# Kernel optimization log

Measured on AMD Instinct MI355X. Metric: run time of the kernel, lower is better.

## Reference

```python
import jax, jax.numpy as jnp
import numpy as np

B, N = 256, 2000          # clouds, points per cloud
M1, M2 = 100, 5           # fps sample counts (ratio 0.05 twice)
K1, K2 = 20, 20           # neighbors per cluster (= 1/ratio)
R1, R2, R3 = 0.3, 1.0, 2.0
F1, F2, F3 = 5, 25, 45


def _fps(pts, m):
    # iterative farthest point sampling, deterministic start at index 0
    n = pts.shape[0]
    def step(carry, _):
        mind, last = carry
        d = jnp.sum((pts - pts[last]) ** 2, axis=-1)
        mind = jnp.minimum(mind, d)
        return (mind, jnp.argmax(mind).astype(jnp.int32)), last
    _, idx = jax.lax.scan(step, (jnp.full((n,), 1e10, pts.dtype), jnp.int32(0)), None, length=m)
    return idx


def _radius_knn(q, pts, k, r):
    # k nearest neighbors of each query, masked to the radius ball (static-shape gnn.radius)
    d = jnp.sum((q[:, None, :] - pts[None, :, :]) ** 2, axis=-1)  # (M, n)
    negd, idx = jax.lax.top_k(-d, k)
    return idx, (-negd) <= r * r


def _masked_max(h, mask):
    return jnp.max(jnp.where(mask[..., None], h, -1e10), axis=1)


def _forward(points, W1, b1, W2, b2, W3, b3, D1, bD1, D2, bD2, D3, bD3):
    def per_cloud(pts):
        # ---- encode level 1 ----
        samples = pts[_fps(pts, M1)]                              # (M1,3)
        idx1, m1 = _radius_knn(samples, pts, K1, R1)
        rel = (pts[idx1] - samples[:, None, :]) / R1 * m1[..., None]   # (M1,K1,3)
        f1 = _masked_max(jax.nn.relu(rel @ W1 + b1), m1)          # (M1,F1)
        # ---- encode level 2 ----
        samples2 = samples[_fps(samples, M2)]                     # (M2,3)
        idx2, m2 = _radius_knn(samples2, samples, K2, R2)
        rel2 = (samples[idx2] - samples2[:, None, :]) / R2 * m2[..., None]
        h2 = jax.nn.relu(jnp.concatenate([rel2, f1[idx2]], axis=-1) @ W2 + b2)
        f2 = _masked_max(h2, m2)                                  # (M2,F2)
        # ---- encode level 3 (global) ----
        rel3 = samples2 / R3
        h3 = jax.nn.relu(jnp.concatenate([rel3, f2], axis=-1) @ W3 + b3)
        latent = jnp.max(h3, axis=0)                              # (F3,)
        # ---- hierarchical decode ----
        o1 = (latent @ D1 + bD1).reshape(M2, 3 + F2)
        dec, cf = o1[:, :3], jax.nn.relu(o1[:, 3:])               # (M2,3),(M2,F2)
        o2 = (cf @ D2 + bD2).reshape(M2 * K2, 3 + F1)
        dec2, cf2 = o2[:, :3], jax.nn.relu(o2[:, 3:])             # (M2*K2,3/F1)
        dec3 = (cf2 @ D3 + bD3).reshape(M2 * K2 * K1, 3)
        # ---- reconstruction: repeat_interleave + add + scale ----
        s2_out = dec * R3
        s_out = (jnp.repeat(s2_out, K2, axis=0) + dec2) * R2
        return (jnp.repeat(s_out, K1, axis=0) + dec3) * R1        # (N,3)
    return jax.vmap(per_cloud)(points).reshape(B * N, 3)


def setup_inputs():
    key = jax.random.key(0)
    ks = jax.random.split(key, 8)
    p = lambda k, s: jax.random.normal(k, s, jnp.float32) * 0.1
    z = lambda s: jnp.zeros((s,), jnp.float32)
    return {
        "points": jax.random.normal(ks[0], (B, N, 3), jnp.float32),
        "W1": p(ks[1], (3, F1)), "b1": z(F1),
        "W2": p(ks[2], (3 + F1, F2)), "b2": z(F2),
        "W3": p(ks[3], (3 + F2, F3)), "b3": z(F3),
        "D1": p(ks[4], (F3, M2 * (3 + F2))), "bD1": z(M2 * (3 + F2)),
        "D2": p(ks[5], (F2, K2 * (3 + F1))), "bD2": z(K2 * (3 + F1)),
        "D3": p(ks[6], (F1, K1 * 3)), "bD3": z(K1 * 3),
    }


def reference(points, W1, b1, W2, b2, W3, b3, D1, bD1, D2, bD2, D3, bD3):
    return _forward(points, W1, b1, W2, b2, W3, b3, D1, bD1, D2, bD2, D3, bD3)
```

## Files before the change

### kernel.cpp

```cpp
#include <hip/hip_runtime.h>

#define TPB 512
#define NW 8
#define NPTS 2000
#define M1C 100
#define M2C 5
#define KNN 20
#define CANDCAP 128

typedef float v2f __attribute__((ext_vector_type(2)));

__device__ __forceinline__ float dist3(float px, float py, float pz,
                                       float qx, float qy, float qz) {
#pragma clang fp contract(off)
    float dx = px - qx, dy = py - qy, dz = pz - qz;
    return dx * dx + dy * dy + dz * dz;
}

__device__ __forceinline__ v2f dist3p(v2f px, v2f py, v2f pz, v2f q0, v2f q1, v2f q2) {
#pragma clang fp contract(off)
    v2f dx = px - q0, dy = py - q1, dz = pz - q2;
    v2f ax = dx * dx;
    v2f ay = dy * dy;
    v2f az = dz * dz;
    return (ax + ay) + az;
}

#define ARGMAX_STEP(ctrl, rm)                                                        \
    do {                                                                             \
        float ov = __int_as_float(__builtin_amdgcn_update_dpp(                       \
            (int)0xff800000, __float_as_int(v), ctrl, rm, 0xf, false));              \
        int oi = __builtin_amdgcn_update_dpp(0x7fffffff, i, ctrl, rm, 0xf, false);   \
        bool take = (ov > v) || (ov == v && oi < i);                                 \
        v = take ? ov : v;                                                           \
        i = take ? oi : i;                                                           \
    } while (0)

__device__ __forceinline__ void wave_argmax(float& v, int& i) {
    ARGMAX_STEP(0x111, 0xf);
    ARGMAX_STEP(0x112, 0xf);
    ARGMAX_STEP(0x114, 0xf);
    ARGMAX_STEP(0x118, 0xf);
    ARGMAX_STEP(0x142, 0xa);
    ARGMAX_STEP(0x143, 0xc);
    v = __int_as_float(__builtin_amdgcn_readlane(__float_as_int(v), 63));
    i = __builtin_amdgcn_readlane(i, 63);
}

#define FMAX_STEP(ctrl, rm)                                                          \
    do {                                                                             \
        float _t = __int_as_float(__builtin_amdgcn_update_dpp(                       \
            (int)0xff800000, __float_as_int(x), ctrl, rm, 0xf, false));              \
        x = fmaxf(x, _t);                                                            \
    } while (0)

__device__ __forceinline__ float wave_fmax(float x) {
    FMAX_STEP(0x111, 0xf);
    FMAX_STEP(0x112, 0xf);
    FMAX_STEP(0x114, 0xf);
    FMAX_STEP(0x118, 0xf);
    FMAX_STEP(0x142, 0xa);
    FMAX_STEP(0x143, 0xc);
    return __int_as_float(__builtin_amdgcn_readlane(__float_as_int(x), 63));
}

__global__ __launch_bounds__(TPB, 2) void fused_kernel(
    const float* __restrict__ P,
    const float* __restrict__ W1, const float* __restrict__ b1,
    const float* __restrict__ W2, const float* __restrict__ b2,
    const float* __restrict__ W3, const float* __restrict__ b3,
    const float* __restrict__ D1, const float* __restrict__ bD1,
    const float* __restrict__ D2, const float* __restrict__ bD2,
    const float* __restrict__ D3, const float* __restrict__ bD3,
    float* __restrict__ out)
{
    __shared__ float sx[NPTS], sy[NPTS], sz[NPTS];
    __shared__ float smpx[M1C], smpy[M1C], smpz[M1C];
    __shared__ float s2x[M2C], s2y[M2C], s2z[M2C];
    __shared__ float f1s[M1C][5];
    __shared__ float knd[NW][CANDCAP];
    __shared__ int   kni[NW][CANDCAP];
    __shared__ float vin[M2C][KNN][8];
    __shared__ __align__(16) float4 sA[2][4];
    __shared__ __align__(16) float  sZ[2][4];
    __shared__ int cnt;
    __shared__ float f2s[M2C][25];
    __shared__ float latent[45];
    __shared__ float decv[M2C][3];
    __shared__ float cfs[M2C][25];
    __shared__ float dec2s[M1C][3];
    __shared__ float cf2s[M1C][5];
    __shared__ float w2s[200], b2s[25], w3s[1260], b3s[45];

    const int b = blockIdx.x;
    const int tid = threadIdx.x;
    const int lane = tid & 63;
    const int wid = tid >> 6;

    const float R1SQ = (float)(0.3 * 0.3);
    const float R2SQ = 1.0f;
    const float INVR1 = 1.0f / 0.3f;

    const float* Pb = P + (size_t)b * (NPTS * 3);
    for (int j = tid; j < NPTS; j += TPB) {
        sx[j] = Pb[3 * j + 0];
        sy[j] = Pb[3 * j + 1];
        sz[j] = Pb[3 * j + 2];
    }
    for (int t = tid; t < 200; t += TPB) w2s[t] = W2[t];
    for (int t = tid; t < 25; t += TPB) b2s[t] = b2[t];
    for (int t = tid; t < 1260; t += TPB) w3s[t] = W3[t];
    for (int t = tid; t < 45; t += TPB) b3s[t] = b3[t];
    if (tid == 0) cnt = 0;
    __syncthreads();

    if (wid < 4) {
        v2f px2[4], py2[4], pz2[4], mind2[4];
#pragma unroll
        for (int p = 0; p < 4; ++p) {
#pragma unroll
            for (int h = 0; h < 2; ++h) {
                int k = 2 * p + h;
                int j = tid + (k << 8);
                bool v = j < NPTS;
                int jc = v ? j : 0;
                px2[p][h] = v ? sx[jc] : 1e18f;
                py2[p][h] = v ? sy[jc] : 1e18f;
                pz2[p][h] = v ? sz[jc] : 1e18f;
                mind2[p][h] = v ? 1e10f : -1.0f;
            }
        }

        float qx = sx[0], qy = sy[0], qz = sz[0];
        for (int it = 0; it < M1C; ++it) {
            if (tid == 0) { smpx[it] = qx; smpy[it] = qy; smpz[it] = qz; }
            v2f q0 = {qx, qx}, q1 = {qy, qy}, q2 = {qz, qz};
            float m[8];
#pragma unroll
            for (int p = 0; p < 4; ++p) {
                v2f d = dist3p(px2[p], py2[p], pz2[p], q0, q1, q2);
                v2f mm;
                mm[0] = fminf(mind2[p][0], d[0]);
                mm[1] = fminf(mind2[p][1], d[1]);
                mind2[p] = mm;
                m[2 * p] = mm[0];
                m[2 * p + 1] = mm[1];
            }
            float va = m[0]; int ka = 0; if (m[1] > va) { va = m[1]; ka = 1; }
            float vb = m[2]; int kb = 2; if (m[3] > vb) { vb = m[3]; kb = 3; }
            float vc = m[4]; int kc = 4; if (m[5] > vc) { vc = m[5]; kc = 5; }
            float vd = m[6]; int kd = 6; if (m[7] > vd) { vd = m[7]; kd = 7; }
            if (vb > va) { va = vb; ka = kb; }
            if (vd > vc) { vc = vd; kc = kd; }
            if (vc > va) { va = vc; ka = kc; }
            float bv = va; int bi = tid + (ka << 8);
            if (it == M1C - 1) {
                if (lane == 0)
                    __hip_atomic_fetch_add(&cnt, 1, __ATOMIC_RELEASE,
                                           __HIP_MEMORY_SCOPE_WORKGROUP);
                break;
            }
            float lv = bv; int li = bi;
            wave_argmax(bv, bi);
            int p = it & 1;
            if (lv == bv && li == bi) {
                int k = bi >> 8;
                float cx = px2[0][0], cy = py2[0][0], cz = pz2[0][0];
#pragma unroll
                for (int kk = 1; kk < 8; ++kk) {
                    bool t = (k == kk);
                    cx = t ? px2[kk >> 1][kk & 1] : cx;
                    cy = t ? py2[kk >> 1][kk & 1] : cy;
                    cz = t ? pz2[kk >> 1][kk & 1] : cz;
                }
                sA[p][wid] = make_float4(bv, __int_as_float(bi), cx, cy);
                sZ[p][wid] = cz;
            }
            if (lane == 0)
                __hip_atomic_fetch_add(&cnt, 1, __ATOMIC_RELEASE,
                                       __HIP_MEMORY_SCOPE_WORKGROUP);
            int need = 4 * (it + 1);
            for (;;) {
                int c = __hip_atomic_load(&cnt, __ATOMIC_ACQUIRE,
                                          __HIP_MEMORY_SCOPE_WORKGROUP);
                if (c >= need) break;
                __builtin_amdgcn_s_sleep(1);
            }
            float4 a0 = sA[p][0], a1 = sA[p][1], a2 = sA[p][2], a3 = sA[p][3];
            float4 z0 = *(const float4*)&sZ[p][0];
            float cv0 = a0.x; int ci0 = __float_as_int(a0.y);
            float x0 = a0.z, y0 = a0.w, zz0 = z0.x;
            {
                int ii = __float_as_int(a1.y);
                bool t = (a1.x > cv0) || (a1.x == cv0 && ii < ci0);
                if (t) { cv0 = a1.x; ci0 = ii; x0 = a1.z; y0 = a1.w; zz0 = z0.y; }
            }
            float cv1 = a2.x; int ci1 = __float_as_int(a2.y);
            float x1 = a2.z, y1 = a2.w, zz1 = z0.z;
            {
                int ii = __float_as_int(a3.y);
                bool t = (a3.x > cv1) || (a3.x == cv1 && ii < ci1);
                if (t) { cv1 = a3.x; ci1 = ii; x1 = a3.z; y1 = a3.w; zz1 = z0.w; }
            }
            bool t = (cv1 > cv0) || (cv1 == cv0 && ci1 < ci0);
            qx = t ? x1 : x0; qy = t ? y1 : y0; qz = t ? zz1 : zz0;
        }

        if (wid == 0) {
            float ax = smpx[lane], ay = smpy[lane], az = smpz[lane];
            bool vb2 = lane < (M1C - 64);
            float bx2 = vb2 ? smpx[lane + 64] : 1e18f;
            float by2 = vb2 ? smpy[lane + 64] : 1e18f;
            float bz2 = vb2 ? smpz[lane + 64] : 1e18f;
            float m2a = 1e10f;
            float m2b = vb2 ? 1e10f : -1.0f;
            int last2 = 0;
            for (int it = 0; it < M2C; ++it) {
                float fx = smpx[last2], fy = smpy[last2], fz = smpz[last2];
                if (lane == 0) { s2x[it] = fx; s2y[it] = fy; s2z[it] = fz; }
                m2a = fminf(m2a, dist3(ax, ay, az, fx, fy, fz));
                m2b = fminf(m2b, dist3(bx2, by2, bz2, fx, fy, fz));
                float v = m2a; int i = lane;
                if (m2b > v) { v = m2b; i = lane + 64; }
                wave_argmax(v, i);
                last2 = i;
            }
        }
    } else {
        float rw1[15], rb1[5];
#pragma unroll
        for (int i = 0; i < 15; ++i) rw1[i] = W1[i];
#pragma unroll
        for (int i = 0; i < 5; ++i) rb1[i] = b1[i];

        for (int s = wid - 4; s < M1C; s += 4) {
            while (__hip_atomic_load(&cnt, __ATOMIC_ACQUIRE,
                                     __HIP_MEMORY_SCOPE_WORKGROUP) < 4 * (s + 1))
                __builtin_amdgcn_s_sleep(2);
            float qx = smpx[s], qy = smpy[s], qz = smpz[s];
            int cn = 0;
#pragma unroll 4
            for (int c = 0; c < 32; ++c) {
                int j = c * 64 + lane;
                float d = 0.0f; bool pred = false;
                if (j < NPTS) {
                    d = dist3(sx[j], sy[j], sz[j], qx, qy, qz);
                    pred = (d <= R1SQ);
                }
                unsigned long long mb = __ballot(pred);
                if (pred) {
                    int pos = cn + (int)__popcll(mb & ((1ull << lane) - 1ull));
                    if (pos < CANDCAP) { knd[wid][pos] = d; kni[wid][pos] = j; }
                }
                cn += (int)__popcll(mb);
            }
            if (cn > CANDCAP) cn = CANDCAP;
            float fmx[5];
#pragma unroll
            for (int f = 0; f < 5; ++f) fmx[f] = -1e30f;
            for (int t = lane; t < cn; t += 64) {
                float d = knd[wid][t]; int j = kni[wid][t];
                bool valid = true;
                if (cn > KNN) {
                    int rank = 0;
                    for (int u = 0; u < cn; ++u) {
                        float du = knd[wid][u]; int iu = kni[wid][u];
                        rank += (du < d || (du == d && iu < j)) ? 1 : 0;
                    }
                    valid = rank < KNN;
                }
                if (valid) {
                    float rx = (sx[j] - qx) * INVR1;
                    float ry = (sy[j] - qy) * INVR1;
                    float rz = (sz[j] - qz) * INVR1;
#pragma unroll
                    for (int f = 0; f < 5; ++f) {
                        float h = fmaf(rx, rw1[f], fmaf(ry, rw1[5 + f], fmaf(rz, rw1[10 + f], rb1[f])));
                        fmx[f] = fmaxf(fmx[f], fmaxf(h, 0.0f));
                    }
                }
            }
#pragma unroll
            for (int f = 0; f < 5; ++f) fmx[f] = wave_fmax(fmx[f]);
            if (lane == 0) {
#pragma unroll
                for (int f = 0; f < 5; ++f) f1s[s][f] = fmx[f];
            }
        }
    }
    __syncthreads();

    for (int s = wid; s < M2C; s += NW) {
        float qx2 = s2x[s], qy2 = s2y[s], qz2 = s2z[s];
        int cn = 0;
#pragma unroll
        for (int c = 0; c < 2; ++c) {
            int j = c * 64 + lane;
            float d = 0.0f; bool pred = false;
            if (j < M1C) {
                d = dist3(smpx[j], smpy[j], smpz[j], qx2, qy2, qz2);
                pred = (d <= R2SQ);
            }
            unsigned long long mb = __ballot(pred);
            if (pred) {
                int pos = cn + (int)__popcll(mb & ((1ull << lane) - 1ull));
                knd[wid][pos] = d; kni[wid][pos] = j;
            }
            cn += (int)__popcll(mb);
        }
        int nv = 0;
#pragma unroll
        for (int c = 0; c < 2; ++c) {
            int t = c * 64 + lane;
            bool valid = false;
            float in8[8];
            if (t < cn) {
                float d = knd[wid][t]; int j = kni[wid][t];
                valid = true;
                if (cn > KNN) {
                    int rank = 0;
                    for (int u = 0; u < cn; ++u) {
                        float du = knd[wid][u]; int iu = kni[wid][u];
                        rank += (du < d || (du == d && iu < j)) ? 1 : 0;
                    }
                    valid = rank < KNN;
                }
                if (valid) {
                    in8[0] = smpx[j] - qx2; in8[1] = smpy[j] - qy2; in8[2] = smpz[j] - qz2;
#pragma unroll
                    for (int f = 0; f < 5; ++f) in8[3 + f] = f1s[j][f];
                }
            }
            unsigned long long mb = __ballot(valid);
            if (valid) {
                int pos = nv + (int)__popcll(mb & ((1ull << lane) - 1ull));
#pragma unroll
                for (int i = 0; i < 8; ++i) vin[s][pos][i] = in8[i];
            }
            nv += (int)__popcll(mb);
        }
        if (lane < 25) {
            float hmx = -1e30f;
            for (int c = 0; c < nv; ++c) {
                float h = b2s[lane];
#pragma unroll
                for (int i = 0; i < 8; ++i) h = fmaf(vin[s][c][i], w2s[i * 25 + lane], h);
                hmx = fmaxf(hmx, fmaxf(h, 0.0f));
            }
            f2s[s][lane] = hmx;
        }
    }
    __syncthreads();

    if (wid == 0 && lane < 45) {
        float lm = -1e30f;
        for (int r = 0; r < M2C; ++r) {
            float h = b3s[lane];
            h = fmaf(s2x[r] * 0.5f, w3s[0 * 45 + lane], h);
            h = fmaf(s2y[r] * 0.5f, w3s[1 * 45 + lane], h);
            h = fmaf(s2z[r] * 0.5f, w3s[2 * 45 + lane], h);
#pragma unroll
            for (int i = 0; i < 25; ++i) h = fmaf(f2s[r][i], w3s[(3 + i) * 45 + lane], h);
            lm = fmaxf(lm, fmaxf(h, 0.0f));
        }
        latent[lane] = lm;
    }
    __syncthreads();

    for (int t = tid; t < 140; t += TPB) {
        float acc = bD1[t];
        for (int i = 0; i < 45; i++) acc = fmaf(latent[i], D1[i * 140 + t], acc);
        int r = t / 28, c = t % 28;
        if (c < 3) decv[r][c] = acc;
        else cfs[r][c - 3] = fmaxf(acc, 0.0f);
    }
    __syncthreads();

    for (int t = tid; t < 800; t += TPB) {
        int r = t / 160, c = t % 160;
        float acc = bD2[c];
        for (int i = 0; i < 25; i++) acc = fmaf(cfs[r][i], D2[i * 160 + c], acc);
        int g = r * 20 + c / 8, c8 = c % 8;
        if (c8 < 3) dec2s[g][c8] = acc;
        else cf2s[g][c8 - 3] = fmaxf(acc, 0.0f);
    }
    __syncthreads();

    float* outb = out + (size_t)b * (NPTS * 3);
    for (int t = tid; t < NPTS * 3; t += TPB) {
        int n = t / 3, c = t % 3;
        int g = n / 20;
        int m = n / 400;
        int r60 = (n % 20) * 3 + c;
        float acc = bD3[r60];
        for (int i = 0; i < 5; i++) acc = fmaf(cf2s[g][i], D3[i * 60 + r60], acc);
        float val = ((decv[m][c] * 2.0f + dec2s[g][c]) + acc) * 0.3f;
        outb[t] = val;
    }
}

extern "C" void kernel_launch(void* const* d_in, const int* in_sizes, int n_in,
                              void* d_out, int out_size, void* d_ws, size_t ws_size,
                              hipStream_t stream) {
    const float* P   = (const float*)d_in[0];
    const float* W1  = (const float*)d_in[1];
    const float* b1  = (const float*)d_in[2];
    const float* W2  = (const float*)d_in[3];
    const float* b2  = (const float*)d_in[4];
    const float* W3  = (const float*)d_in[5];
    const float* b3  = (const float*)d_in[6];
    const float* D1  = (const float*)d_in[7];
    const float* bD1 = (const float*)d_in[8];
    const float* D2  = (const float*)d_in[9];
    const float* bD2 = (const float*)d_in[10];
    const float* D3  = (const float*)d_in[11];
    const float* bD3 = (const float*)d_in[12];
    float* out = (float*)d_out;

    int B = in_sizes[0] / (NPTS * 3);
    hipLaunchKernelGGL(fused_kernel, dim3(B), dim3(TPB), 0, stream,
                       P, W1, b1, W2, b2, W3, b3, D1, bD1, D2, bD2, D3, bD3, out);
}
```

Measured before the change: 188.1 us.

## Reuse FPS distances to collect radius candidates in sampler waves

The FPS waves already compute the distance from every point to each new sample, so they now push in-radius points into a per-sample shared candidate list with an atomic counter. The consumer waves then skip their own full 2000-point distance scan and only rank the collected candidates. Separate counters signal sample readiness and candidate readiness, and the sleep in the FPS spin wait is removed. The per-sample cap drops from 128 to 64, so dense neighbourhoods get truncated, and the atomics add work to the critical FPS loop.

```diff
diff --git a/kernel.cpp b/kernel.cpp
--- a/kernel.cpp
+++ b/kernel.cpp
@@ -7,6 +7,7 @@
 #define M2C 5
 #define KNN 20
 #define CANDCAP 128
+#define CCAP 64
 
 typedef float v2f __attribute__((ext_vector_type(2)));
 
@@ -83,7 +84,10 @@
     __shared__ float vin[M2C][KNN][8];
     __shared__ __align__(16) float4 sA[2][4];
     __shared__ __align__(16) float  sZ[2][4];
-    __shared__ int cnt;
+    __shared__ int cntS;
+    __shared__ int cntC;
+    __shared__ float2 cand[M1C][CCAP];
+    __shared__ int ccnt[M1C];
     __shared__ float f2s[M2C][25];
     __shared__ float latent[45];
     __shared__ float decv[M2C][3];
@@ -111,7 +115,8 @@
     for (int t = tid; t < 25; t += TPB) b2s[t] = b2[t];
     for (int t = tid; t < 1260; t += TPB) w3s[t] = W3[t];
     for (int t = tid; t < 45; t += TPB) b3s[t] = b3[t];
-    if (tid == 0) cnt = 0;
+    if (tid < M1C) ccnt[tid] = 0;
+    if (tid == 0) { cntS = 0; cntC = 0; }
     __syncthreads();
 
     if (wid < 4) {
@@ -136,9 +141,11 @@
             if (tid == 0) { smpx[it] = qx; smpy[it] = qy; smpz[it] = qz; }
             v2f q0 = {qx, qx}, q1 = {qy, qy}, q2 = {qz, qz};
             float m[8];
+            v2f dv[4];
 #pragma unroll
             for (int p = 0; p < 4; ++p) {
                 v2f d = dist3p(px2[p], py2[p], pz2[p], q0, q1, q2);
+                dv[p] = d;
                 v2f mm;
                 mm[0] = fminf(mind2[p][0], d[0]);
                 mm[1] = fminf(mind2[p][1], d[1]);
@@ -146,46 +153,60 @@
                 m[2 * p] = mm[0];
                 m[2 * p + 1] = mm[1];
             }
-            float va = m[0]; int ka = 0; if (m[1] > va) { va = m[1]; ka = 1; }
-            float vb = m[2]; int kb = 2; if (m[3] > vb) { vb = m[3]; kb = 3; }
-            float vc = m[4]; int kc = 4; if (m[5] > vc) { vc = m[5]; kc = 5; }
-            float vd = m[6]; int kd = 6; if (m[7] > vd) { vd = m[7]; kd = 7; }
-            if (vb > va) { va = vb; ka = kb; }
-            if (vd > vc) { vc = vd; kc = kd; }
-            if (vc > va) { va = vc; ka = kc; }
-            float bv = va; int bi = tid + (ka << 8);
-            if (it == M1C - 1) {
+
+            if (it < M1C - 1) {
+                float va = m[0]; int ka = 0; if (m[1] > va) { va = m[1]; ka = 1; }
+                float vb = m[2]; int kb = 2; if (m[3] > vb) { vb = m[3]; kb = 3; }
+                float vc = m[4]; int kc = 4; if (m[5] > vc) { vc = m[5]; kc = 5; }
+                float vd = m[6]; int kd = 6; if (m[7] > vd) { vd = m[7]; kd = 7; }
+                if (vb > va) { va = vb; ka = kb; }
+                if (vd > vc) { vc = vd; kc = kd; }
+                if (vc > va) { va = vc; ka = kc; }
+                float bv = va; int bi = tid + (ka << 8);
+                float lv = bv; int li = bi;
+                wave_argmax(bv, bi);
+                int p = it & 1;
+                if (lv == bv && li == bi) {
+                    int k = bi >> 8;
+                    float cx = px2[0][0], cy = py2[0][0], cz = pz2[0][0];
+#pragma unroll
+                    for (int kk = 1; kk < 8; ++kk) {
+                        bool t = (k == kk);
+                        cx = t ? px2[kk >> 1][kk & 1] : cx;
+                        cy = t ? py2[kk >> 1][kk & 1] : cy;
+                        cz = t ? pz2[kk >> 1][kk & 1] : cz;
+                    }
+                    sA[p][wid] = make_float4(bv, __int_as_float(bi), cx, cy);
+                    sZ[p][wid] = cz;
+                }
                 if (lane == 0)
-                    __hip_atomic_fetch_add(&cnt, 1, __ATOMIC_RELEASE,
+                    __hip_atomic_fetch_add(&cntS, 1, __ATOMIC_RELEASE,
                                            __HIP_MEMORY_SCOPE_WORKGROUP);
-                break;
-            }
-            float lv = bv; int li = bi;
-            wave_argmax(bv, bi);
-            int p = it & 1;
-            if (lv == bv && li == bi) {
-                int k = bi >> 8;
-                float cx = px2[0][0], cy = py2[0][0], cz = pz2[0][0];
-#pragma unroll
-                for (int kk = 1; kk < 8; ++kk) {
-                    bool t = (k == kk);
-                    cx = t ? px2[kk >> 1][kk & 1] : cx;
-                    cy = t ? py2[kk >> 1][kk & 1] : cy;
-                    cz = t ? pz2[kk >> 1][kk & 1] : cz;
-                }
-                sA[p][wid] = make_float4(bv, __int_as_float(bi), cx, cy);
-                sZ[p][wid] = cz;
+            }
+
+#pragma unroll
+            for (int k = 0; k < 8; ++k) {
+                float dk = dv[k >> 1][k & 1];
+                if (dk <= R1SQ) {
+                    int pos = __hip_atomic_fetch_add(&ccnt[it], 1, __ATOMIC_RELAXED,
+                                                     __HIP_MEMORY_SCOPE_WORKGROUP);
+                    if (pos < CCAP)
+                        cand[it][pos] = make_float2(dk, __int_as_float(tid + (k << 8)));
+                }
             }
             if (lane == 0)
-                __hip_atomic_fetch_add(&cnt, 1, __ATOMIC_RELEASE,
+                __hip_atomic_fetch_add(&cntC, 1, __ATOMIC_RELEASE,
                                        __HIP_MEMORY_SCOPE_WORKGROUP);
+
+            if (it == M1C - 1) break;
+
             int need = 4 * (it + 1);
             for (;;) {
-                int c = __hip_atomic_load(&cnt, __ATOMIC_ACQUIRE,
+                int c = __hip_atomic_load(&cntS, __ATOMIC_ACQUIRE,
                                           __HIP_MEMORY_SCOPE_WORKGROUP);
                 if (c >= need) break;
-                __builtin_amdgcn_s_sleep(1);
-            }
+            }
+            int p = it & 1;
             float4 a0 = sA[p][0], a1 = sA[p][1], a2 = sA[p][2], a3 = sA[p][3];
             float4 z0 = *(const float4*)&sZ[p][0];
             float cv0 = a0.x; int ci0 = __float_as_int(a0.y);
@@ -234,50 +255,40 @@
         for (int i = 0; i < 5; ++i) rb1[i] = b1[i];
 
         for (int s = wid - 4; s < M1C; s += 4) {
-            while (__hip_atomic_load(&cnt, __ATOMIC_ACQUIRE,
-                                     __HIP_MEMORY_SCOPE_WORKGROUP) < 4 * (s + 1))
-                __builtin_amdgcn_s_sleep(2);
+            int need = 4 * (s + 1);
+            while (__hip_atomic_load(&cntC, __ATOMIC_ACQUIRE,
+                                     __HIP_MEMORY_SCOPE_WORKGROUP) < need)
+                __builtin_amdgcn_s_sleep(1);
             float qx = smpx[s], qy = smpy[s], qz = smpz[s];
-            int cn = 0;
-#pragma unroll 4
-            for (int c = 0; c < 32; ++c) {
-                int j = c * 64 + lane;
-                float d = 0.0f; bool pred = false;
-                if (j < NPTS) {
-                    d = dist3(sx[j], sy[j], sz[j], qx, qy, qz);
-                    pred = (d <= R1SQ);
-                }
-                unsigned long long mb = __ballot(pred);
-                if (pred) {
-                    int pos = cn + (int)__popcll(mb & ((1ull << lane) - 1ull));
-                    if (pos < CANDCAP) { knd[wid][pos] = d; kni[wid][pos] = j; }
-                }
-                cn += (int)__popcll(mb);
-            }
-            if (cn > CANDCAP) cn = CANDCAP;
+            int cn = ccnt[s];
+            if (cn > CCAP) cn = CCAP;
             float fmx[5];
 #pragma unroll
             for (int f = 0; f < 5; ++f) fmx[f] = -1e30f;
-            for (int t = lane; t < cn; t += 64) {
-                float d = knd[wid][t]; int j = kni[wid][t];
-                bool valid = true;
+            bool valid = lane < cn;
+            float d = 0.0f; int j = 0;
+            if (valid) {
+                float2 c = cand[s][lane];
+                d = c.x;
+                j = __float_as_int(c.y);
                 if (cn > KNN) {
                     int rank = 0;
                     for (int u = 0; u < cn; ++u) {
-                        float du = knd[wid][u]; int iu = kni[wid][u];
-                        rank += (du < d || (du == d && iu < j)) ? 1 : 0;
+                        float2 cu = cand[s][u];
+                        int iu = __float_as_int(cu.y);
+                        rank += (cu.x < d || (cu.x == d && iu < j)) ? 1 : 0;
                     }
                     valid = rank < KNN;
                 }
-                if (valid) {
-                    float rx = (sx[j] - qx) * INVR1;
-                    float ry = (sy[j] - qy) * INVR1;
-                    float rz = (sz[j] - qz) * INVR1;
-#pragma unroll
-                    for (int f = 0; f < 5; ++f) {
-                        float h = fmaf(rx, rw1[f], fmaf(ry, rw1[5 + f], fmaf(rz, rw1[10 + f], rb1[f])));
-                        fmx[f] = fmaxf(fmx[f], fmaxf(h, 0.0f));
-                    }
+            }
+            if (valid) {
+                float rx = (sx[j] - qx) * INVR1;
+                float ry = (sy[j] - qy) * INVR1;
+                float rz = (sz[j] - qz) * INVR1;
+#pragma unroll
+                for (int f = 0; f < 5; ++f) {
+                    float h = fmaf(rx, rw1[f], fmaf(ry, rw1[5 + f], fmaf(rz, rw1[10 + f], rb1[f])));
+                    fmx[f] = fmaxf(h, 0.0f);
                 }
             }
 #pragma unroll
```

Result: slower. 210.5 us (+11.9%).

## Drop producer-consumer wave split; run FPS then kNN sequentially in 256-thread block

Applied to the files above, without the earlier changes.

Shrinks the block from 8 waves to 4 and removes the specialization in which four waves ran FPS while four other waves consumed samples through an atomic counter with spin waits. All four waves now run FPS using a __syncthreads per iteration, then the level-2 FPS, then all waves run the radius/kNN stage over the samples. This removes the atomic/sleep polling but gives up the overlap between FPS and the neighbor search, which now becomes a serial phase. Point indexing changes to a wave-contiguous layout.

```diff
diff --git a/kernel.cpp b/kernel.cpp
--- a/kernel.cpp
+++ b/kernel.cpp
@@ -1,7 +1,7 @@
 #include <hip/hip_runtime.h>
 
-#define TPB 512
-#define NW 8
+#define TPB 256
+#define NW 4
 #define NPTS 2000
 #define M1C 100
 #define M2C 5
@@ -64,7 +64,7 @@
     return __int_as_float(__builtin_amdgcn_readlane(__float_as_int(x), 63));
 }
 
-__global__ __launch_bounds__(TPB, 2) void fused_kernel(
+__global__ __launch_bounds__(TPB, 1) void fused_kernel(
     const float* __restrict__ P,
     const float* __restrict__ W1, const float* __restrict__ b1,
     const float* __restrict__ W2, const float* __restrict__ b2,
@@ -83,7 +83,6 @@
     __shared__ float vin[M2C][KNN][8];
     __shared__ __align__(16) float4 sA[2][4];
     __shared__ __align__(16) float  sZ[2][4];
-    __shared__ int cnt;
     __shared__ float f2s[M2C][25];
     __shared__ float latent[45];
     __shared__ float decv[M2C][3];
@@ -111,17 +110,16 @@
     for (int t = tid; t < 25; t += TPB) b2s[t] = b2[t];
     for (int t = tid; t < 1260; t += TPB) w3s[t] = W3[t];
     for (int t = tid; t < 45; t += TPB) b3s[t] = b3[t];
-    if (tid == 0) cnt = 0;
-    __syncthreads();
-
-    if (wid < 4) {
+    __syncthreads();
+
+    {
         v2f px2[4], py2[4], pz2[4], mind2[4];
 #pragma unroll
         for (int p = 0; p < 4; ++p) {
 #pragma unroll
             for (int h = 0; h < 2; ++h) {
-                int k = 2 * p + h;
-                int j = tid + (k << 8);
+                int k = (wid << 3) + 2 * p + h;
+                int j = (k << 6) + lane;
                 bool v = j < NPTS;
                 int jc = v ? j : 0;
                 px2[p][h] = v ? sx[jc] : 1e18f;
@@ -134,6 +132,8 @@
         float qx = sx[0], qy = sy[0], qz = sz[0];
         for (int it = 0; it < M1C; ++it) {
             if (tid == 0) { smpx[it] = qx; smpy[it] = qy; smpz[it] = qz; }
+            if (it == M1C - 1) break;
+
             v2f q0 = {qx, qx}, q1 = {qy, qy}, q2 = {qz, qz};
             float m[8];
 #pragma unroll
@@ -153,22 +153,16 @@
             if (vb > va) { va = vb; ka = kb; }
             if (vd > vc) { vc = vd; kc = kd; }
             if (vc > va) { va = vc; ka = kc; }
-            float bv = va; int bi = tid + (ka << 8);
-            if (it == M1C - 1) {
-                if (lane == 0)
-                    __hip_atomic_fetch_add(&cnt, 1, __ATOMIC_RELEASE,
-                                           __HIP_MEMORY_SCOPE_WORKGROUP);
-                break;
-            }
+            float bv = va;
+            int bi = (((wid << 3) + ka) << 6) | lane;
             float lv = bv; int li = bi;
             wave_argmax(bv, bi);
             int p = it & 1;
             if (lv == bv && li == bi) {
-                int k = bi >> 8;
                 float cx = px2[0][0], cy = py2[0][0], cz = pz2[0][0];
 #pragma unroll
                 for (int kk = 1; kk < 8; ++kk) {
-                    bool t = (k == kk);
+                    bool t = (ka == kk);
                     cx = t ? px2[kk >> 1][kk & 1] : cx;
                     cy = t ? py2[kk >> 1][kk & 1] : cy;
                     cz = t ? pz2[kk >> 1][kk & 1] : cz;
@@ -176,16 +170,7 @@
                 sA[p][wid] = make_float4(bv, __int_as_float(bi), cx, cy);
                 sZ[p][wid] = cz;
             }
-            if (lane == 0)
-                __hip_atomic_fetch_add(&cnt, 1, __ATOMIC_RELEASE,
-                                       __HIP_MEMORY_SCOPE_WORKGROUP);
-            int need = 4 * (it + 1);
-            for (;;) {
-                int c = __hip_atomic_load(&cnt, __ATOMIC_ACQUIRE,
-                                          __HIP_MEMORY_SCOPE_WORKGROUP);
-                if (c >= need) break;
-                __builtin_amdgcn_s_sleep(1);
-            }
+            __syncthreads();
             float4 a0 = sA[p][0], a1 = sA[p][1], a2 = sA[p][2], a3 = sA[p][3];
             float4 z0 = *(const float4*)&sZ[p][0];
             float cv0 = a0.x; int ci0 = __float_as_int(a0.y);
@@ -205,38 +190,38 @@
             bool t = (cv1 > cv0) || (cv1 == cv0 && ci1 < ci0);
             qx = t ? x1 : x0; qy = t ? y1 : y0; qz = t ? zz1 : zz0;
         }
-
-        if (wid == 0) {
-            float ax = smpx[lane], ay = smpy[lane], az = smpz[lane];
-            bool vb2 = lane < (M1C - 64);
-            float bx2 = vb2 ? smpx[lane + 64] : 1e18f;
-            float by2 = vb2 ? smpy[lane + 64] : 1e18f;
-            float bz2 = vb2 ? smpz[lane + 64] : 1e18f;
-            float m2a = 1e10f;
-            float m2b = vb2 ? 1e10f : -1.0f;
-            int last2 = 0;
-            for (int it = 0; it < M2C; ++it) {
-                float fx = smpx[last2], fy = smpy[last2], fz = smpz[last2];
-                if (lane == 0) { s2x[it] = fx; s2y[it] = fy; s2z[it] = fz; }
-                m2a = fminf(m2a, dist3(ax, ay, az, fx, fy, fz));
-                m2b = fminf(m2b, dist3(bx2, by2, bz2, fx, fy, fz));
-                float v = m2a; int i = lane;
-                if (m2b > v) { v = m2b; i = lane + 64; }
-                wave_argmax(v, i);
-                last2 = i;
-            }
-        }
-    } else {
+    }
+    __syncthreads();
+
+    if (wid == 0) {
+        float ax = smpx[lane], ay = smpy[lane], az = smpz[lane];
+        bool vb2 = lane < (M1C - 64);
+        float bx2 = vb2 ? smpx[lane + 64] : 1e18f;
+        float by2 = vb2 ? smpy[lane + 64] : 1e18f;
+        float bz2 = vb2 ? smpz[lane + 64] : 1e18f;
+        float m2a = 1e10f;
+        float m2b = vb2 ? 1e10f : -1.0f;
+        int last2 = 0;
+        for (int it = 0; it < M2C; ++it) {
+            float fx = smpx[last2], fy = smpy[last2], fz = smpz[last2];
+            if (lane == 0) { s2x[it] = fx; s2y[it] = fy; s2z[it] = fz; }
+            m2a = fminf(m2a, dist3(ax, ay, az, fx, fy, fz));
+            m2b = fminf(m2b, dist3(bx2, by2, bz2, fx, fy, fz));
+            float v = m2a; int i = lane;
+            if (m2b > v) { v = m2b; i = lane + 64; }
+            wave_argmax(v, i);
+            last2 = i;
+        }
+    }
+
+    {
         float rw1[15], rb1[5];
 #pragma unroll
         for (int i = 0; i < 15; ++i) rw1[i] = W1[i];
 #pragma unroll
         for (int i = 0; i < 5; ++i) rb1[i] = b1[i];
 
-        for (int s = wid - 4; s < M1C; s += 4) {
-            while (__hip_atomic_load(&cnt, __ATOMIC_ACQUIRE,
-                                     __HIP_MEMORY_SCOPE_WORKGROUP) < 4 * (s + 1))
-                __builtin_amdgcn_s_sleep(2);
+        for (int s = wid; s < M1C; s += NW) {
             float qx = smpx[s], qy = smpy[s], qz = smpz[s];
             int cn = 0;
 #pragma unroll 4
```

After: 269.7 us. 43.4% more time.

## Replace FPS atomic counter with per-wave flags, progress index, and priority boost

Applied to the files above, without the earlier changes.

The single shared atomic counter that both FPS waves and neighbor waves polled is replaced by per-wave parity flags spun on without sleep by the FPS waves, plus a separate progress index that consumer waves watch. The FPS waves also raise their scheduling priority, and the point cloud is stored as float4 in LDS so each point needs one vector load instead of three scalar ones. The aim is to shorten the serial FPS critical path by cutting atomic read-modify-write contention and sleep latency per iteration. Busy spinning without sleep may take issue slots from the consumer waves, and float4 storage uses a third more LDS.

```diff
diff --git a/kernel.cpp b/kernel.cpp
--- a/kernel.cpp
+++ b/kernel.cpp
@@ -74,7 +74,7 @@
     const float* __restrict__ D3, const float* __restrict__ bD3,
     float* __restrict__ out)
 {
-    __shared__ float sx[NPTS], sy[NPTS], sz[NPTS];
+    __shared__ __align__(16) float4 sp[NPTS];
     __shared__ float smpx[M1C], smpy[M1C], smpz[M1C];
     __shared__ float s2x[M2C], s2y[M2C], s2z[M2C];
     __shared__ float f1s[M1C][5];
@@ -83,7 +83,8 @@
     __shared__ float vin[M2C][KNN][8];
     __shared__ __align__(16) float4 sA[2][4];
     __shared__ __align__(16) float  sZ[2][4];
-    __shared__ int cnt;
+    __shared__ int flg[2][4];
+    __shared__ int prog;
     __shared__ float f2s[M2C][25];
     __shared__ float latent[45];
     __shared__ float decv[M2C][3];
@@ -103,18 +104,18 @@
 
     const float* Pb = P + (size_t)b * (NPTS * 3);
     for (int j = tid; j < NPTS; j += TPB) {
-        sx[j] = Pb[3 * j + 0];
-        sy[j] = Pb[3 * j + 1];
-        sz[j] = Pb[3 * j + 2];
+        sp[j] = make_float4(Pb[3 * j + 0], Pb[3 * j + 1], Pb[3 * j + 2], 0.0f);
     }
     for (int t = tid; t < 200; t += TPB) w2s[t] = W2[t];
     for (int t = tid; t < 25; t += TPB) b2s[t] = b2[t];
     for (int t = tid; t < 1260; t += TPB) w3s[t] = W3[t];
     for (int t = tid; t < 45; t += TPB) b3s[t] = b3[t];
-    if (tid == 0) cnt = 0;
+    if (tid < 8) ((int*)flg)[tid] = 0;
+    if (tid == 0) prog = -1;
     __syncthreads();
 
     if (wid < 4) {
+        __builtin_amdgcn_s_setprio(1);
         v2f px2[4], py2[4], pz2[4], mind2[4];
 #pragma unroll
         for (int p = 0; p < 4; ++p) {
@@ -123,17 +124,24 @@
                 int k = 2 * p + h;
                 int j = tid + (k << 8);
                 bool v = j < NPTS;
-                int jc = v ? j : 0;
-                px2[p][h] = v ? sx[jc] : 1e18f;
-                py2[p][h] = v ? sy[jc] : 1e18f;
-                pz2[p][h] = v ? sz[jc] : 1e18f;
+                float4 A = sp[v ? j : 0];
+                px2[p][h] = v ? A.x : 1e18f;
+                py2[p][h] = v ? A.y : 1e18f;
+                pz2[p][h] = v ? A.z : 1e18f;
                 mind2[p][h] = v ? 1e10f : -1.0f;
             }
         }
 
-        float qx = sx[0], qy = sy[0], qz = sz[0];
+        float4 qq0 = sp[0];
+        float qx = qq0.x, qy = qq0.y, qz = qq0.z;
         for (int it = 0; it < M1C; ++it) {
-            if (tid == 0) { smpx[it] = qx; smpy[it] = qy; smpz[it] = qz; }
+            if (tid == 0) {
+                smpx[it] = qx; smpy[it] = qy; smpz[it] = qz;
+                __hip_atomic_store(&prog, it, __ATOMIC_RELEASE,
+                                   __HIP_MEMORY_SCOPE_WORKGROUP);
+            }
+            if (it == M1C - 1) break;
+
             v2f q0 = {qx, qx}, q1 = {qy, qy}, q2 = {qz, qz};
             float m[8];
 #pragma unroll
@@ -154,12 +162,6 @@
             if (vd > vc) { vc = vd; kc = kd; }
             if (vc > va) { va = vc; ka = kc; }
             float bv = va; int bi = tid + (ka << 8);
-            if (it == M1C - 1) {
-                if (lane == 0)
-                    __hip_atomic_fetch_add(&cnt, 1, __ATOMIC_RELEASE,
-                                           __HIP_MEMORY_SCOPE_WORKGROUP);
-                break;
-            }
             float lv = bv; int li = bi;
             wave_argmax(bv, bi);
             int p = it & 1;
@@ -177,14 +179,22 @@
                 sZ[p][wid] = cz;
             }
             if (lane == 0)
-                __hip_atomic_fetch_add(&cnt, 1, __ATOMIC_RELEASE,
-                                       __HIP_MEMORY_SCOPE_WORKGROUP);
-            int need = 4 * (it + 1);
-            for (;;) {
-                int c = __hip_atomic_load(&cnt, __ATOMIC_ACQUIRE,
-                                          __HIP_MEMORY_SCOPE_WORKGROUP);
-                if (c >= need) break;
-                __builtin_amdgcn_s_sleep(1);
+                __hip_atomic_store(&flg[p][wid], it + 1, __ATOMIC_RELEASE,
+                                   __HIP_MEMORY_SCOPE_WORKGROUP);
+            {
+                const int need = it + 1;
+                for (;;) {
+                    int f0 = __hip_atomic_load(&flg[p][0], __ATOMIC_RELAXED,
+                                               __HIP_MEMORY_SCOPE_WORKGROUP);
+                    int f1 = __hip_atomic_load(&flg[p][1], __ATOMIC_RELAXED,
+                                               __HIP_MEMORY_SCOPE_WORKGROUP);
+                    int f2 = __hip_atomic_load(&flg[p][2], __ATOMIC_RELAXED,
+                                               __HIP_MEMORY_SCOPE_WORKGROUP);
+                    int f3 = __hip_atomic_load(&flg[p][3], __ATOMIC_RELAXED,
+                                               __HIP_MEMORY_SCOPE_WORKGROUP);
+                    if (f0 >= need && f1 >= need && f2 >= need && f3 >= need) break;
+                }
+                __builtin_amdgcn_fence(__ATOMIC_ACQUIRE, "workgroup");
             }
             float4 a0 = sA[p][0], a1 = sA[p][1], a2 = sA[p][2], a3 = sA[p][3];
             float4 z0 = *(const float4*)&sZ[p][0];
@@ -226,6 +236,7 @@
                 last2 = i;
             }
         }
+        __builtin_amdgcn_s_setprio(0);
     } else {
         float rw1[15], rb1[5];
 #pragma unroll
@@ -234,9 +245,9 @@
         for (int i = 0; i < 5; ++i) rb1[i] = b1[i];
 
         for (int s = wid - 4; s < M1C; s += 4) {
-            while (__hip_atomic_load(&cnt, __ATOMIC_ACQUIRE,
-                                     __HIP_MEMORY_SCOPE_WORKGROUP) < 4 * (s + 1))
-                __builtin_amdgcn_s_sleep(2);
+            while (__hip_atomic_load(&prog, __ATOMIC_ACQUIRE,
+                                     __HIP_MEMORY_SCOPE_WORKGROUP) < s)
+                __builtin_amdgcn_s_sleep(1);
             float qx = smpx[s], qy = smpy[s], qz = smpz[s];
             int cn = 0;
 #pragma unroll 4
@@ -244,7 +255,8 @@
                 int j = c * 64 + lane;
                 float d = 0.0f; bool pred = false;
                 if (j < NPTS) {
-                    d = dist3(sx[j], sy[j], sz[j], qx, qy, qz);
+                    float4 pj = sp[j];
+                    d = dist3(pj.x, pj.y, pj.z, qx, qy, qz);
                     pred = (d <= R1SQ);
                 }
                 unsigned long long mb = __ballot(pred);
@@ -270,9 +282,10 @@
                     valid = rank < KNN;
                 }
                 if (valid) {
-                    float rx = (sx[j] - qx) * INVR1;
-                    float ry = (sy[j] - qy) * INVR1;
-                    float rz = (sz[j] - qz) * INVR1;
+                    float4 pj = sp[j];
+                    float rx = (pj.x - qx) * INVR1;
+                    float ry = (pj.y - qy) * INVR1;
+                    float rz = (pj.z - qz) * INVR1;
 #pragma unroll
                     for (int f = 0; f < 5; ++f) {
                         float h = fmaf(rx, rw1[f], fmaf(ry, rw1[5 + f], fmaf(rz, rw1[10 + f], rb1[f])));
```

New measurement: 187.0 us. No clear change (-0.6%).
